# Kernel tuning notes

Measured on AMD Instinct MI355X. Metric: run time of the kernel, lower is better.

Reference implementation:

```python
import jax, jax.numpy as jnp
import numpy as np

HEADS = 16

def setup_inputs() -> dict:
    key = jax.random.key(0)
    ks = jax.random.split(key, 5)
    B, S, D = 4, 2048, 1024
    scale = 1.0 / np.sqrt(D)
    return {
        "x": jax.random.normal(ks[0], (B, S, D), dtype=jnp.float32),
        "WQ": jax.random.normal(ks[1], (D, D), dtype=jnp.float32) * scale,
        "WK": jax.random.normal(ks[2], (D, D), dtype=jnp.float32) * scale,
        "WV": jax.random.normal(ks[3], (D, D), dtype=jnp.float32) * scale,
        "WO": jax.random.normal(ks[4], (D, D), dtype=jnp.float32) * scale,
    }

def reference(x, WQ, WK, WV, WO):
    B, S, D = x.shape
    H = HEADS
    dh = D // H
    Q = x @ WQ  # [B,S,D]
    K = x @ WK
    V = x @ WV
    # tf.stack(tf.split(., heads, axis=2)) == reshape to [B,S,H,dh] then move H first
    def to_heads(t):
        return t.reshape(B, S, H, dh).transpose(2, 0, 1, 3)  # [H,B,S,dh]
    Qh, Kh, Vh = to_heads(Q), to_heads(K), to_heads(V)
    # NOTE: original scales by sqrt(n_dims) (full model dim), not sqrt(head_dim)
    scores = jnp.einsum("hbqd,hbkd->hbqk", Qh, Kh) / jnp.sqrt(jnp.asarray(D, x.dtype))
    probs = jax.nn.softmax(scores, axis=-1)  # [H,B,Sq,Sk]
    ctx = jnp.einsum("hbqk,hbkd->hbqd", probs, Vh)  # [H,B,S,dh]
    # concat(unstack(axis=0), axis=-1): heads back to contiguous chunks of last dim
    out = ctx.transpose(1, 2, 0, 3).reshape(B, S, D)
    return out @ WO
```

## Files before the change

### kernel.cpp

```cpp
#include <hip/hip_runtime.h>
#include <stdint.h>

typedef unsigned short u16;
typedef __bf16 bf16x8 __attribute__((ext_vector_type(8)));
typedef float f32x4 __attribute__((ext_vector_type(4)));
typedef float f32x16 __attribute__((ext_vector_type(16)));
typedef unsigned short u16x8 __attribute__((ext_vector_type(8)));
typedef unsigned short u16x4 __attribute__((ext_vector_type(4)));

#define HD 16
#define BB 4
#define SS 2048
#define DD 1024
#define DH 64

#if __has_builtin(__builtin_amdgcn_exp2f)
#define EXP2(x) __builtin_amdgcn_exp2f(x)
#else
#define EXP2(x) exp2f(x)
#endif

__device__ __forceinline__ u16 f2bf(float f) {
  union { float f; uint32_t u; } v; v.f = f;
  uint32_t u = v.u;
  return (u16)((u + 0x7FFFu + ((u >> 16) & 1u)) >> 16);
}

__device__ __forceinline__ u16 bfbits(float f) {
  union { __bf16 h; u16 u; } c;
  c.h = (__bf16)f;
  return c.u;
}

__device__ __forceinline__ uint32_t cvtpk(float lo, float hi) {
  uint32_t r;
  asm("v_cvt_pk_bf16_f32 %0, %1, %2" : "=v"(r) : "v"(lo), "v"(hi));
  return r;
}

__device__ __forceinline__ void gl2lds16(const void* g, void* l) {
  __builtin_amdgcn_global_load_lds(
      (const __attribute__((address_space(1))) void*)g,
      (__attribute__((address_space(3))) void*)l, 16, 0, 0);
}

__global__ __launch_bounds__(256) void cast_x_kernel(const float* __restrict__ src,
                                                     u16* __restrict__ dst, int n4) {
  int i = blockIdx.x * 256 + threadIdx.x;
  if (i >= n4) return;
  float4 v = ((const float4*)src)[i];
  u16x4 o;
  o.x = f2bf(v.x); o.y = f2bf(v.y); o.z = f2bf(v.z); o.w = f2bf(v.w);
  ((u16x4*)dst)[i] = o;
}

__global__ __launch_bounds__(256) void wtrans4_kernel(const float* __restrict__ WQ,
                                                      const float* __restrict__ WK,
                                                      const float* __restrict__ WV,
                                                      const float* __restrict__ WO,
                                                      u16* __restrict__ wcat,
                                                      u16* __restrict__ wot, float qscale) {
  __shared__ u16 tile[64][65];
  const int z = blockIdx.z;
  const float* src = (z == 0) ? WQ : (z == 1) ? WK : (z == 2) ? WV : WO;
  u16* dst = (z < 3) ? wcat + (size_t)z * 1024 * 1024 : wot;
  const float scale = (z == 0) ? qscale : 1.0f;
  const int bx = blockIdx.x * 64;
  const int by = blockIdx.y * 64;
  const int t = threadIdx.x;
  const int c = t & 63, r0 = t >> 6;
#pragma unroll
  for (int r = r0; r < 64; r += 4)
    tile[r][c] = f2bf(src[(size_t)(by + r) * 1024 + bx + c] * scale);
  __syncthreads();
#pragma unroll
  for (int r = r0; r < 64; r += 4)
    dst[(size_t)(bx + r) * 1024 + by + c] = tile[c][r];
}

__global__ __launch_bounds__(256) void vtrans_kernel(const u16* __restrict__ qkv,
                                                     u16* __restrict__ vt) {
  __shared__ u16 tile[64][65];
  const int s0 = blockIdx.x * 64;
  const int h = blockIdx.y;
  const int b = blockIdx.z;
  const int t = threadIdx.x;
  const int c = t & 63, r0 = t >> 6;
#pragma unroll
  for (int r = r0; r < 64; r += 4)
    tile[r][c] = qkv[(size_t)(b * SS + s0 + r) * 3072 + 2048 + h * DH + c];
  __syncthreads();
#pragma unroll
  for (int r = r0; r < 64; r += 4)
    vt[((size_t)(b * HD + h) * DH + r) * SS + s0 + c] = tile[c][r];
}

template <int OUT_BF16>
__global__ __launch_bounds__(256) void gemm_nt_kernel(const u16* __restrict__ A,
                                                      const u16* __restrict__ Bt,
                                                      void* __restrict__ Cv,
                                                      int M, int N, int K) {
  __shared__ __attribute__((aligned(16))) u16 As[128 * 64];
  __shared__ __attribute__((aligned(16))) u16 Bs[128 * 64];
  const int t = threadIdx.x;
  const int lane = t & 63;
  const int w = t >> 6;
  const int m0 = blockIdx.y * 128;
  const int n0 = blockIdx.x * 128;

  f32x16 acc[2][2] = {};

  const int srow = t >> 3;
  const int cpos = t & 7;
  const int scc = cpos ^ (srow & 7);
  const int wm = (w >> 1) * 64;
  const int wn = (w & 1) * 64;
  const int l31 = lane & 31;
  const int kh = lane >> 5;

  for (int k0 = 0; k0 < K; k0 += 64) {
#pragma unroll
    for (int p = 0; p < 4; ++p) {
      int row = p * 32 + srow;
      gl2lds16(A + (size_t)(m0 + row) * K + k0 + scc * 8, (char*)As + p * 4096 + w * 1024);
      gl2lds16(Bt + (size_t)(n0 + row) * K + k0 + scc * 8, (char*)Bs + p * 4096 + w * 1024);
    }
    __syncthreads();

#pragma unroll
    for (int ks = 0; ks < 4; ++ks) {
      bf16x8 af[2], bfr[2];
#pragma unroll
      for (int i = 0; i < 2; ++i) {
        int ra = wm + i * 32 + l31;
        af[i] = *(const bf16x8*)(As + ra * 64 + (((ks * 2 + kh) ^ (ra & 7)) * 8));
        int rb = wn + i * 32 + l31;
        bfr[i] = *(const bf16x8*)(Bs + rb * 64 + (((ks * 2 + kh) ^ (rb & 7)) * 8));
      }
#pragma unroll
      for (int i = 0; i < 2; ++i)
#pragma unroll
        for (int j = 0; j < 2; ++j)
          acc[i][j] = __builtin_amdgcn_mfma_f32_32x32x16_bf16(af[i], bfr[j], acc[i][j], 0, 0, 0);
    }
    __syncthreads();
  }

#pragma unroll
  for (int i = 0; i < 2; ++i)
#pragma unroll
    for (int j = 0; j < 2; ++j)
#pragma unroll
      for (int rg = 0; rg < 16; ++rg) {
        int gr = m0 + wm + i * 32 + (rg & 3) + ((rg >> 2) * 8) + 4 * kh;
        int gc = n0 + wn + j * 32 + l31;
        float v = acc[i][j][rg];
        if (OUT_BF16)
          ((u16*)Cv)[(size_t)gr * N + gc] = f2bf(v);
        else
          ((float*)Cv)[(size_t)gr * N + gc] = v;
      }
}

__global__ __launch_bounds__(256) void attn_kernel(const u16* __restrict__ qkv,
                                                   const u16* __restrict__ vt,
                                                   u16* __restrict__ ctx) {
  __shared__ __attribute__((aligned(16))) u16 KV[2 * 64 * 64];
  u16* Ks = KV;
  u16* Vs = KV + 4096;

  const int t = threadIdx.x;
  const int lane = t & 63;
  const int w = t >> 6;
  const int q0 = blockIdx.x * 64;
  const int h = blockIdx.y;
  const int b = blockIdx.z;

  const int srow = t >> 3;
  const int cpos = t & 7;
  const size_t qkv_row0 = (size_t)(b * SS) * 3072;
  const size_t vtbase = ((size_t)(b * HD + h) * DH) * SS;

  const int lr = lane & 15, kg = lane >> 4;

  bf16x8 aq[2];
#pragma unroll
  for (int ks = 0; ks < 2; ++ks)
    aq[ks] = *(const bf16x8*)(qkv + qkv_row0 + (size_t)(q0 + w * 16 + lr) * 3072 +
                              h * DH + ks * 32 + kg * 8);

  f32x4 ot[4] = {};
  float l_p = 0.f;

  for (int k0 = 0; k0 < SS; k0 += 64) {
#pragma unroll
    for (int p = 0; p < 2; ++p) {
      int r = p * 32 + srow;
      int cc = cpos ^ ((r & 7) ^ (((r >> 3) & 3) << 1));
      gl2lds16(qkv + qkv_row0 + (size_t)(k0 + r) * 3072 + 1024 + h * DH + cc * 8,
               (char*)Ks + p * 4096 + w * 1024);
      gl2lds16(vt + vtbase + (size_t)r * SS + k0 + cc * 8,
               (char*)Vs + p * 4096 + w * 1024);
    }
    __syncthreads();

    f32x4 c4[4] = {};
#pragma unroll
    for (int ks = 0; ks < 2; ++ks) {
#pragma unroll
      for (int nt = 0; nt < 4; ++nt) {
        int jr = ((lr >> 2) << 3) + (lr & 3) + ((nt & 1) << 5) + ((nt >> 1) << 2);
        int scj = (jr & 7) ^ (((jr >> 3) & 3) << 1);
        bf16x8 ak = *(const bf16x8*)(Ks + jr * 64 + (((ks * 4 + kg) ^ scj) * 8));
        c4[nt] = __builtin_amdgcn_mfma_f32_16x16x32_bf16(ak, aq[ks], c4[nt], 0, 0, 0);
      }
    }

#pragma unroll
    for (int nt = 0; nt < 4; ++nt)
#pragma unroll
      for (int r = 0; r < 4; ++r)
        c4[nt][r] = EXP2(c4[nt][r]);
    l_p += ((c4[0][0] + c4[0][1]) + (c4[0][2] + c4[0][3])) +
           ((c4[1][0] + c4[1][1]) + (c4[1][2] + c4[1][3])) +
           ((c4[2][0] + c4[2][1]) + (c4[2][2] + c4[2][3])) +
           ((c4[3][0] + c4[3][1]) + (c4[3][2] + c4[3][3]));

    union { uint32_t u[4]; bf16x8 b; } bp[2];
#pragma unroll
    for (int ks = 0; ks < 2; ++ks) {
      bp[ks].u[0] = cvtpk(c4[ks][0], c4[ks][1]);
      bp[ks].u[1] = cvtpk(c4[ks][2], c4[ks][3]);
      bp[ks].u[2] = cvtpk(c4[2 + ks][0], c4[2 + ks][1]);
      bp[ks].u[3] = cvtpk(c4[2 + ks][2], c4[2 + ks][3]);
    }

#pragma unroll
    for (int ks = 0; ks < 2; ++ks) {
#pragma unroll
      for (int dt = 0; dt < 4; ++dt) {
        int vr = dt * 16 + lr;
        int scv = (vr & 7) ^ (((vr >> 3) & 3) << 1);
        bf16x8 av = *(const bf16x8*)(Vs + vr * 64 + (((ks * 4 + kg) ^ scv) * 8));
        ot[dt] = __builtin_amdgcn_mfma_f32_16x16x32_bf16(av, bp[ks].b, ot[dt], 0, 0, 0);
      }
    }
    __syncthreads();
  }

  l_p += __shfl_xor(l_p, 16, 64);
  l_p += __shfl_xor(l_p, 32, 64);
  const float inv_l = 1.0f / l_p;

  u16* Es = KV;
#pragma unroll
  for (int dt = 0; dt < 4; ++dt) {
    u16x4 pv;
#pragma unroll
    for (int r = 0; r < 4; ++r) pv[r] = bfbits(ot[dt][r] * inv_l);
    *(u16x4*)(Es + (w * 16 + lr) * 72 + dt * 16 + kg * 4) = pv;
  }

  const int rr = lane >> 3;
  const int cc8 = lane & 7;
#pragma unroll
  for (int p = 0; p < 2; ++p) {
    int row = p * 8 + rr;
    u16x8 vv = *(const u16x8*)(Es + (w * 16 + row) * 72 + cc8 * 8);
    *(u16x8*)(ctx + (size_t)(b * SS + q0 + w * 16 + row) * DD + h * DH + cc8 * 8) = vv;
  }
}

extern "C" void kernel_launch(void* const* d_in, const int* in_sizes, int n_in,
                              void* d_out, int out_size, void* d_ws, size_t ws_size,
                              hipStream_t stream) {
  (void)in_sizes; (void)n_in; (void)out_size; (void)ws_size;
  const float* x = (const float*)d_in[0];
  const float* WQ = (const float*)d_in[1];
  const float* WK = (const float*)d_in[2];
  const float* WV = (const float*)d_in[3];
  const float* WO = (const float*)d_in[4];

  char* ws = (char*)d_ws;
  u16* xb = (u16*)ws;            ws += (size_t)8192 * 1024 * 2;
  u16* wcat = (u16*)ws;          ws += (size_t)3072 * 1024 * 2;
  u16* wot = (u16*)ws;           ws += (size_t)1024 * 1024 * 2;
  u16* qkv = (u16*)ws;           ws += (size_t)8192 * 3072 * 2;
  u16* vt = (u16*)ws;            ws += (size_t)BB * HD * DH * SS * 2;
  u16* ctx = xb;

  const float QSCALE = 0.03125f * 1.4426950408889634f;

  cast_x_kernel<<<dim3(8192), dim3(256), 0, stream>>>(x, xb, 2097152);
  wtrans4_kernel<<<dim3(16, 16, 4), dim3(256), 0, stream>>>(WQ, WK, WV, WO, wcat, wot, QSCALE);

  gemm_nt_kernel<1><<<dim3(24, 64), dim3(256), 0, stream>>>(xb, wcat, (void*)qkv, 8192, 3072, 1024);
  vtrans_kernel<<<dim3(32, 16, 4), dim3(256), 0, stream>>>(qkv, vt);
  attn_kernel<<<dim3(32, 16, 4), dim3(256), 0, stream>>>(qkv, vt, ctx);
  gemm_nt_kernel<0><<<dim3(8, 64), dim3(256), 0, stream>>>(ctx, wot, d_out, 8192, 1024, 1024);
}
```

Before: 292.3 us.

## Switch attention to 32x32x16 MFMA with 128-query tiles per block

The attention kernel now gives each wave 32 query rows instead of 16, so a block covers 128 queries and the grid halves. It uses 32x32x16 bf16 MFMA tiles instead of 16x16x32, with a new K row permutation, a simpler XOR swizzle and a new epilogue layout. Each K/V tile loaded into LDS is now reused across twice as many queries, cutting global K/V traffic and barrier count per query. The cost is more accumulator registers per thread (bounded by launch_bounds 256,4) and fewer blocks in flight.

```diff
diff --git a/kernel.cpp b/kernel.cpp
--- a/kernel.cpp
+++ b/kernel.cpp
@@ -162,17 +162,17 @@
       }
 }
 
-__global__ __launch_bounds__(256) void attn_kernel(const u16* __restrict__ qkv,
-                                                   const u16* __restrict__ vt,
-                                                   u16* __restrict__ ctx) {
-  __shared__ __attribute__((aligned(16))) u16 KV[2 * 64 * 64];
-  u16* Ks = KV;
-  u16* Vs = KV + 4096;
+__global__ __launch_bounds__(256, 4) void attn_kernel(const u16* __restrict__ qkv,
+                                                      const u16* __restrict__ vt,
+                                                      u16* __restrict__ ctx) {
+  __shared__ __attribute__((aligned(16))) u16 SMEM[9216];
+  u16* Ks = SMEM;
+  u16* Vs = SMEM + 4096;
 
   const int t = threadIdx.x;
   const int lane = t & 63;
   const int w = t >> 6;
-  const int q0 = blockIdx.x * 64;
+  const int q0 = blockIdx.x * 128;
   const int h = blockIdx.y;
   const int b = blockIdx.z;
 
@@ -181,22 +181,24 @@
   const size_t qkv_row0 = (size_t)(b * SS) * 3072;
   const size_t vtbase = ((size_t)(b * HD + h) * DH) * SS;
 
-  const int lr = lane & 15, kg = lane >> 4;
-
-  bf16x8 aq[2];
-#pragma unroll
-  for (int ks = 0; ks < 2; ++ks)
-    aq[ks] = *(const bf16x8*)(qkv + qkv_row0 + (size_t)(q0 + w * 16 + lr) * 3072 +
-                              h * DH + ks * 32 + kg * 8);
-
-  f32x4 ot[4] = {};
+  const int l31 = lane & 31;
+  const int kh = lane >> 5;
+  const int p31 = (l31 & 19) | ((l31 & 4) << 1) | ((l31 & 8) >> 1);
+
+  bf16x8 aq[4];
+#pragma unroll
+  for (int ks = 0; ks < 4; ++ks)
+    aq[ks] = *(const bf16x8*)(qkv + qkv_row0 + (size_t)(q0 + w * 32 + l31) * 3072 +
+                              h * DH + ks * 16 + kh * 8);
+
+  f32x16 ot[2] = {};
   float l_p = 0.f;
 
   for (int k0 = 0; k0 < SS; k0 += 64) {
 #pragma unroll
     for (int p = 0; p < 2; ++p) {
       int r = p * 32 + srow;
-      int cc = cpos ^ ((r & 7) ^ (((r >> 3) & 3) << 1));
+      int cc = cpos ^ (r & 7);
       gl2lds16(qkv + qkv_row0 + (size_t)(k0 + r) * 3072 + 1024 + h * DH + cc * 8,
                (char*)Ks + p * 4096 + w * 1024);
       gl2lds16(vt + vtbase + (size_t)r * SS + k0 + cc * 8,
@@ -204,70 +206,72 @@
     }
     __syncthreads();
 
-    f32x4 c4[4] = {};
-#pragma unroll
-    for (int ks = 0; ks < 2; ++ks) {
-#pragma unroll
-      for (int nt = 0; nt < 4; ++nt) {
-        int jr = ((lr >> 2) << 3) + (lr & 3) + ((nt & 1) << 5) + ((nt >> 1) << 2);
-        int scj = (jr & 7) ^ (((jr >> 3) & 3) << 1);
-        bf16x8 ak = *(const bf16x8*)(Ks + jr * 64 + (((ks * 4 + kg) ^ scj) * 8));
-        c4[nt] = __builtin_amdgcn_mfma_f32_16x16x32_bf16(ak, aq[ks], c4[nt], 0, 0, 0);
+    f32x16 c2[2] = {};
+#pragma unroll
+    for (int ks = 0; ks < 4; ++ks) {
+#pragma unroll
+      for (int tt = 0; tt < 2; ++tt) {
+        int jr = tt * 32 + p31;
+        bf16x8 ak = *(const bf16x8*)(Ks + jr * 64 + (((ks * 2 + kh) ^ (jr & 7)) * 8));
+        c2[tt] = __builtin_amdgcn_mfma_f32_32x32x16_bf16(ak, aq[ks], c2[tt], 0, 0, 0);
       }
     }
 
 #pragma unroll
-    for (int nt = 0; nt < 4; ++nt)
-#pragma unroll
-      for (int r = 0; r < 4; ++r)
-        c4[nt][r] = EXP2(c4[nt][r]);
-    l_p += ((c4[0][0] + c4[0][1]) + (c4[0][2] + c4[0][3])) +
-           ((c4[1][0] + c4[1][1]) + (c4[1][2] + c4[1][3])) +
-           ((c4[2][0] + c4[2][1]) + (c4[2][2] + c4[2][3])) +
-           ((c4[3][0] + c4[3][1]) + (c4[3][2] + c4[3][3]));
-
-    union { uint32_t u[4]; bf16x8 b; } bp[2];
-#pragma unroll
-    for (int ks = 0; ks < 2; ++ks) {
-      bp[ks].u[0] = cvtpk(c4[ks][0], c4[ks][1]);
-      bp[ks].u[1] = cvtpk(c4[ks][2], c4[ks][3]);
-      bp[ks].u[2] = cvtpk(c4[2 + ks][0], c4[2 + ks][1]);
-      bp[ks].u[3] = cvtpk(c4[2 + ks][2], c4[2 + ks][3]);
-    }
-
-#pragma unroll
-    for (int ks = 0; ks < 2; ++ks) {
-#pragma unroll
-      for (int dt = 0; dt < 4; ++dt) {
-        int vr = dt * 16 + lr;
-        int scv = (vr & 7) ^ (((vr >> 3) & 3) << 1);
-        bf16x8 av = *(const bf16x8*)(Vs + vr * 64 + (((ks * 4 + kg) ^ scv) * 8));
-        ot[dt] = __builtin_amdgcn_mfma_f32_16x16x32_bf16(av, bp[ks].b, ot[dt], 0, 0, 0);
+    for (int tt = 0; tt < 2; ++tt)
+#pragma unroll
+      for (int r = 0; r < 16; ++r)
+        c2[tt][r] = EXP2(c2[tt][r]);
+    {
+      float s0 = 0.f, s1 = 0.f;
+#pragma unroll
+      for (int r = 0; r < 16; ++r) { s0 += c2[0][r]; s1 += c2[1][r]; }
+      l_p += s0 + s1;
+    }
+
+    union { uint32_t u[4]; bf16x8 b; } bp[4];
+#pragma unroll
+    for (int tt = 0; tt < 2; ++tt)
+#pragma unroll
+      for (int hf = 0; hf < 2; ++hf)
+#pragma unroll
+        for (int i = 0; i < 4; ++i)
+          bp[tt * 2 + hf].u[i] =
+              cvtpk(c2[tt][hf * 8 + 2 * i], c2[tt][hf * 8 + 2 * i + 1]);
+
+#pragma unroll
+    for (int ks = 0; ks < 4; ++ks) {
+#pragma unroll
+      for (int dt = 0; dt < 2; ++dt) {
+        int vr = dt * 32 + l31;
+        bf16x8 av = *(const bf16x8*)(Vs + vr * 64 + (((ks * 2 + kh) ^ (vr & 7)) * 8));
+        ot[dt] = __builtin_amdgcn_mfma_f32_32x32x16_bf16(av, bp[ks].b, ot[dt], 0, 0, 0);
       }
     }
     __syncthreads();
   }
 
-  l_p += __shfl_xor(l_p, 16, 64);
   l_p += __shfl_xor(l_p, 32, 64);
   const float inv_l = 1.0f / l_p;
 
-  u16* Es = KV;
-#pragma unroll
-  for (int dt = 0; dt < 4; ++dt) {
-    u16x4 pv;
-#pragma unroll
-    for (int r = 0; r < 4; ++r) pv[r] = bfbits(ot[dt][r] * inv_l);
-    *(u16x4*)(Es + (w * 16 + lr) * 72 + dt * 16 + kg * 4) = pv;
-  }
+  u16* Es = SMEM;
+#pragma unroll
+  for (int dt = 0; dt < 2; ++dt)
+#pragma unroll
+    for (int rq = 0; rq < 4; ++rq) {
+      u16x4 pv;
+#pragma unroll
+      for (int i = 0; i < 4; ++i) pv[i] = bfbits(ot[dt][rq * 4 + i] * inv_l);
+      *(u16x4*)(Es + (w * 32 + l31) * 72 + dt * 32 + rq * 8 + kh * 4) = pv;
+    }
 
   const int rr = lane >> 3;
   const int cc8 = lane & 7;
 #pragma unroll
-  for (int p = 0; p < 2; ++p) {
-    int row = p * 8 + rr;
-    u16x8 vv = *(const u16x8*)(Es + (w * 16 + row) * 72 + cc8 * 8);
-    *(u16x8*)(ctx + (size_t)(b * SS + q0 + w * 16 + row) * DD + h * DH + cc8 * 8) = vv;
+  for (int p = 0; p < 4; ++p) {
+    int row = w * 32 + p * 8 + rr;
+    u16x8 vv = *(const u16x8*)(Es + row * 72 + cc8 * 8);
+    *(u16x8*)(ctx + (size_t)(b * SS + q0 + row) * DD + h * DH + cc8 * 8) = vv;
   }
 }
 
@@ -296,6 +300,6 @@
 
   gemm_nt_kernel<1><<<dim3(24, 64), dim3(256), 0, stream>>>(xb, wcat, (void*)qkv, 8192, 3072, 1024);
   vtrans_kernel<<<dim3(32, 16, 4), dim3(256), 0, stream>>>(qkv, vt);
-  attn_kernel<<<dim3(32, 16, 4), dim3(256), 0, stream>>>(qkv, vt, ctx);
+  attn_kernel<<<dim3(16, 16, 4), dim3(256), 0, stream>>>(qkv, vt, ctx);
   gemm_nt_kernel<0><<<dim3(8, 64), dim3(256), 0, stream>>>(ctx, wot, d_out, 8192, 1024, 1024);
 }
```

Measured after the change: 273.8 us. 6.3% less time.
